# Kernel optimization log

Measured on AMD Instinct MI355X. Metric: run time of the kernel, lower is better.

Reference implementation:

```python
import jax, jax.numpy as jnp
import numpy as np

BN_EPS = 1e-5


def setup_inputs() -> dict:
    key = jax.random.key(0)
    ks = jax.random.split(key, 6)
    n, c, h, w = 16, 256, 80, 80
    mip = max(8, c // 32)  # reduction=32 -> mip=8
    x = jax.random.normal(ks[0], (n, c, h, w), dtype=jnp.float32)
    # 1x1 conv weights (bias=False), stored as [out_ch, in_ch]
    w_fc = jax.random.normal(ks[1], (mip, c), dtype=jnp.float32) * (1.0 / np.sqrt(c))
    w_h = jax.random.normal(ks[2], (c, mip), dtype=jnp.float32) * (1.0 / np.sqrt(mip))
    w_w = jax.random.normal(ks[3], (c, mip), dtype=jnp.float32) * (1.0 / np.sqrt(mip))
    # BatchNorm2d(mip) inference params
    bn_gamma = jnp.ones((mip,), dtype=jnp.float32)
    bn_beta = jnp.zeros((mip,), dtype=jnp.float32)
    bn_mean = jax.random.normal(ks[4], (mip,), dtype=jnp.float32) * 0.1
    bn_var = jax.random.uniform(ks[5], (mip,), dtype=jnp.float32, minval=0.5, maxval=1.5)
    return {"x": x, "w_fc": w_fc, "bn_gamma": bn_gamma, "bn_beta": bn_beta,
            "bn_mean": bn_mean, "bn_var": bn_var, "w_h": w_h, "w_w": w_w}


def reference(x, w_fc, bn_gamma, bn_beta, bn_mean, bn_var, w_h, w_w):
    n, c, h, w = x.shape
    # Adaptive pools: pool_h -> mean over W (n,c,h); pool_w -> mean over H (n,c,w)
    x_h = jnp.mean(x, axis=3)  # (n, c, h)
    x_w = jnp.mean(x, axis=2)  # (n, c, w)
    # concat along the length axis (equiv. to torch cat on dim=2 after permute)
    y = jnp.concatenate([x_h, x_w], axis=2)  # (n, c, h+w)
    # fc: 1x1 conv c->mip + BN (inference) + SiLU
    y = jnp.einsum('mc,ncl->nml', w_fc, y)  # (n, mip, h+w)
    inv = bn_gamma / jnp.sqrt(bn_var + BN_EPS)
    y = y * inv[None, :, None] + (bn_beta - bn_mean * inv)[None, :, None]
    y = y * jax.nn.sigmoid(y)  # SiLU
    y_h, y_w = y[:, :, :h], y[:, :, h:]  # (n, mip, h), (n, mip, w)
    a_h = jax.nn.sigmoid(jnp.einsum('cm,nml->ncl', w_h, y_h))  # (n, c, h)
    a_w = jax.nn.sigmoid(jnp.einsum('cm,nml->ncl', w_w, y_w))  # (n, c, w)
    return x * a_h[:, :, :, None] * a_w[:, :, None, :]
```

## Files before the change

kernel.cpp:

```cpp
#include <hip/hip_runtime.h>

#define N_   16
#define C_   256
#define H_   80
#define W_   80
#define MIP_ 8
#define L_   160

typedef float f32x4 __attribute__((ext_vector_type(4)));

__global__ __launch_bounds__(320) void pool_kernel(const float* __restrict__ x,
                                                   float* __restrict__ pooled) {
    __shared__ float lds_row[H_][21];
    __shared__ f32x4 lds_col[16][20];
    const int b  = blockIdx.x;
    const int t  = threadIdx.x;
    const int c4 = t % 20;
    const int rg = t / 20;

    const f32x4* xv = reinterpret_cast<const f32x4*>(x + (size_t)b * (H_ * W_));
    f32x4 colacc = {0.f, 0.f, 0.f, 0.f};
    #pragma unroll
    for (int k = 0; k < 5; ++k) {
        f32x4 q = xv[t + 320 * k];
        colacc += q;
        lds_row[rg + 16 * k][c4] = q.x + q.y + q.z + q.w;
    }
    lds_col[rg][c4] = colacc;
    __syncthreads();

    float* outp = pooled + (size_t)b * L_;
    if (t < H_) {
        float s = 0.f;
        #pragma unroll
        for (int j = 0; j < 20; ++j) s += lds_row[t][j];
        outp[t] = s * (1.0f / (float)W_);
    } else if (t >= 128 && t < 128 + 20) {
        const int j = t - 128;
        f32x4 s = lds_col[0][j];
        #pragma unroll
        for (int r = 1; r < 16; ++r) s += lds_col[r][j];
        s *= (1.0f / (float)H_);
        *reinterpret_cast<f32x4*>(outp + H_ + 4 * j) = s;
    }
}

__global__ __launch_bounds__(256) void mid_kernel(const float* __restrict__ pooled,
                                                  const float* __restrict__ w_fc,
                                                  const float* __restrict__ g,
                                                  const float* __restrict__ be,
                                                  const float* __restrict__ mu,
                                                  const float* __restrict__ va,
                                                  float* __restrict__ y_out) {
    __shared__ float red[4 * MIP_];
    const int b    = blockIdx.x;
    const int n    = b / L_;
    const int l    = b - n * L_;
    const int c    = threadIdx.x;
    const int lane = c & 63;
    const int wid  = c >> 6;

    const float p = pooled[((size_t)n * C_ + c) * L_ + l];

    #pragma unroll
    for (int m = 0; m < MIP_; ++m) {
        float v = w_fc[m * C_ + c] * p;
        #pragma unroll
        for (int off = 32; off > 0; off >>= 1) v += __shfl_down(v, off, 64);
        if (lane == 0) red[wid * MIP_ + m] = v;
    }
    __syncthreads();

    if (c < MIP_) {
        float y   = red[c] + red[MIP_ + c] + red[2 * MIP_ + c] + red[3 * MIP_ + c];
        float inv = g[c] * rsqrtf(va[c] + 1e-5f);
        y = y * inv + (be[c] - mu[c] * inv);
        y_out[(size_t)b * MIP_ + c] = y / (1.0f + expf(-y));
    }
}

__global__ __launch_bounds__(256) void apply_kernel(const float* __restrict__ x,
                                                    const float* __restrict__ y,
                                                    const float* __restrict__ w_h,
                                                    const float* __restrict__ w_w,
                                                    float* __restrict__ out) {
    __shared__ float lah[4][H_];
    __shared__ float law[4][W_];
    const int b  = blockIdx.x;
    const int n  = b >> 6;
    const int c0 = (b & 63) << 2;
    const int t  = threadIdx.x;

    #pragma unroll
    for (int pass = 0; pass < 3; ++pass) {
        int idx = t + pass * 256;
        if (idx < 4 * L_) {
            int ch = idx / L_;
            int l  = idx - ch * L_;
            int c  = c0 + ch;
            const float4* yp = reinterpret_cast<const float4*>(y + ((size_t)n * L_ + l) * MIP_);
            const float4* wp = reinterpret_cast<const float4*>(((l < H_) ? w_h : w_w) + c * MIP_);
            float4 y0 = yp[0], y1 = yp[1];
            float4 w0 = wp[0], w1 = wp[1];
            float s = y0.x * w0.x + y0.y * w0.y + y0.z * w0.z + y0.w * w0.w
                    + y1.x * w1.x + y1.y * w1.y + y1.z * w1.z + y1.w * w1.w;
            float gate = 1.0f / (1.0f + expf(-s));
            if (l < H_) lah[ch][l] = gate; else law[ch][l - H_] = gate;
        }
    }
    __syncthreads();

    const float4* xv = reinterpret_cast<const float4*>(x + ((size_t)n * C_ + c0) * (H_ * W_));
    f32x4*        ov = reinterpret_cast<f32x4*>(out + ((size_t)n * C_ + c0) * (H_ * W_));
    #pragma unroll
    for (int it = 0; it < 25; ++it) {
        int v     = t + it * 256;
        int plane = v / 1600;
        int vv    = v - plane * 1600;
        int row   = vv / 20;
        int col0  = (vv - row * 20) * 4;
        float4 q  = xv[v];
        const float ah = lah[plane][row];
        const float* lw = &law[plane][col0];
        f32x4 o;
        o.x = q.x * ah * lw[0];
        o.y = q.y * ah * lw[1];
        o.z = q.z * ah * lw[2];
        o.w = q.w * ah * lw[3];
        __builtin_nontemporal_store(o, &ov[v]);
    }
}

extern "C" void kernel_launch(void* const* d_in, const int* in_sizes, int n_in,
                              void* d_out, int out_size, void* d_ws, size_t ws_size,
                              hipStream_t stream) {
    const float* x    = (const float*)d_in[0];
    const float* w_fc = (const float*)d_in[1];
    const float* g    = (const float*)d_in[2];
    const float* be   = (const float*)d_in[3];
    const float* mu   = (const float*)d_in[4];
    const float* va   = (const float*)d_in[5];
    const float* w_h  = (const float*)d_in[6];
    const float* w_w  = (const float*)d_in[7];
    float* out = (float*)d_out;

    float* pooled = (float*)d_ws;
    float* y      = pooled + (size_t)N_ * C_ * L_;

    pool_kernel <<<N_ * C_,     320, 0, stream>>>(x, pooled);
    mid_kernel  <<<N_ * L_,     256, 0, stream>>>(pooled, w_fc, g, be, mu, va, y);
    apply_kernel<<<N_ * C_ / 4, 256, 0, stream>>>(x, y, w_h, w_w, out);
}
```

Before: 219.8 us.

## Transpose pooled buffer and compute fc per position with one thread

The pool kernel now writes pooled means transposed as [n][l][c] instead of [n][c][l]. The mid kernel changes from one block per (n,l) with shuffle reductions to one block per batch, where each thread computes all 8 fc outputs for one position by walking 256 contiguous channels with vector loads. This removes the cross-wave reductions, the shared-memory sync and the strided gather of pooled data. In exchange the pool kernel's stores become scattered, and the mid kernel launches only 16 blocks, so it may run latency-bound on very few compute units.

```diff
diff --git a/kernel.cpp b/kernel.cpp
--- a/kernel.cpp
+++ b/kernel.cpp
@@ -10,10 +10,12 @@
 typedef float f32x4 __attribute__((ext_vector_type(4)));
 
 __global__ __launch_bounds__(320) void pool_kernel(const float* __restrict__ x,
-                                                   float* __restrict__ pooled) {
+                                                   float* __restrict__ pooled_t) {
     __shared__ float lds_row[H_][21];
     __shared__ f32x4 lds_col[16][20];
     const int b  = blockIdx.x;
+    const int n  = b >> 8;
+    const int c  = b & 255;
     const int t  = threadIdx.x;
     const int c4 = t % 20;
     const int rg = t / 20;
@@ -29,54 +31,62 @@
     lds_col[rg][c4] = colacc;
     __syncthreads();
 
-    float* outp = pooled + (size_t)b * L_;
+    float* outb = pooled_t + (size_t)n * (L_ * C_) + c;
     if (t < H_) {
         float s = 0.f;
         #pragma unroll
         for (int j = 0; j < 20; ++j) s += lds_row[t][j];
-        outp[t] = s * (1.0f / (float)W_);
+        outb[t * C_] = s * (1.0f / (float)W_);
     } else if (t >= 128 && t < 128 + 20) {
         const int j = t - 128;
         f32x4 s = lds_col[0][j];
         #pragma unroll
         for (int r = 1; r < 16; ++r) s += lds_col[r][j];
         s *= (1.0f / (float)H_);
-        *reinterpret_cast<f32x4*>(outp + H_ + 4 * j) = s;
+        outb[(H_ + 4 * j    ) * C_] = s.x;
+        outb[(H_ + 4 * j + 1) * C_] = s.y;
+        outb[(H_ + 4 * j + 2) * C_] = s.z;
+        outb[(H_ + 4 * j + 3) * C_] = s.w;
     }
 }
 
-__global__ __launch_bounds__(256) void mid_kernel(const float* __restrict__ pooled,
+__global__ __launch_bounds__(192) void mid_kernel(const float* __restrict__ pooled_t,
                                                   const float* __restrict__ w_fc,
                                                   const float* __restrict__ g,
                                                   const float* __restrict__ be,
                                                   const float* __restrict__ mu,
                                                   const float* __restrict__ va,
                                                   float* __restrict__ y_out) {
-    __shared__ float red[4 * MIP_];
-    const int b    = blockIdx.x;
-    const int n    = b / L_;
-    const int l    = b - n * L_;
-    const int c    = threadIdx.x;
-    const int lane = c & 63;
-    const int wid  = c >> 6;
+    const int n = blockIdx.x;
+    const int t = threadIdx.x;
+    if (t >= L_) return;
 
-    const float p = pooled[((size_t)n * C_ + c) * L_ + l];
+    const f32x4* row = reinterpret_cast<const f32x4*>(pooled_t + ((size_t)n * L_ + t) * C_);
+    const f32x4* wv  = reinterpret_cast<const f32x4*>(w_fc);
 
+    float acc[MIP_] = {0.f, 0.f, 0.f, 0.f, 0.f, 0.f, 0.f, 0.f};
+    #pragma unroll 8
+    for (int c4 = 0; c4 < 64; ++c4) {
+        const f32x4 p = row[c4];
+        #pragma unroll
+        for (int m = 0; m < MIP_; ++m) {
+            const f32x4 w4 = wv[m * 64 + c4];
+            acc[m] += p.x * w4.x + p.y * w4.y + p.z * w4.z + p.w * w4.w;
+        }
+    }
+
+    f32x4 o0, o1;
     #pragma unroll
     for (int m = 0; m < MIP_; ++m) {
-        float v = w_fc[m * C_ + c] * p;
-        #pragma unroll
-        for (int off = 32; off > 0; off >>= 1) v += __shfl_down(v, off, 64);
-        if (lane == 0) red[wid * MIP_ + m] = v;
+        const float inv = g[m] * rsqrtf(va[m] + 1e-5f);
+        float s = acc[m] * inv + (be[m] - mu[m] * inv);
+        s = s / (1.0f + expf(-s));
+        if (m < 4) { (m == 0) ? (o0.x = s) : (m == 1) ? (o0.y = s) : (m == 2) ? (o0.z = s) : (o0.w = s); }
+        else       { (m == 4) ? (o1.x = s) : (m == 5) ? (o1.y = s) : (m == 6) ? (o1.z = s) : (o1.w = s); }
     }
-    __syncthreads();
-
-    if (c < MIP_) {
-        float y   = red[c] + red[MIP_ + c] + red[2 * MIP_ + c] + red[3 * MIP_ + c];
-        float inv = g[c] * rsqrtf(va[c] + 1e-5f);
-        y = y * inv + (be[c] - mu[c] * inv);
-        y_out[(size_t)b * MIP_ + c] = y / (1.0f + expf(-y));
-    }
+    f32x4* yp = reinterpret_cast<f32x4*>(y_out + ((size_t)n * L_ + t) * MIP_);
+    yp[0] = o0;
+    yp[1] = o1;
 }
 
 __global__ __launch_bounds__(256) void apply_kernel(const float* __restrict__ x,
@@ -144,10 +154,10 @@
     const float* w_w  = (const float*)d_in[7];
     float* out = (float*)d_out;
 
-    float* pooled = (float*)d_ws;
-    float* y      = pooled + (size_t)N_ * C_ * L_;
+    float* pooled_t = (float*)d_ws;
+    float* y        = pooled_t + (size_t)N_ * L_ * C_;
 
-    pool_kernel <<<N_ * C_,     320, 0, stream>>>(x, pooled);
-    mid_kernel  <<<N_ * L_,     256, 0, stream>>>(pooled, w_fc, g, be, mu, va, y);
+    pool_kernel <<<N_ * C_,     320, 0, stream>>>(x, pooled_t);
+    mid_kernel  <<<N_,          192, 0, stream>>>(pooled_t, w_fc, g, be, mu, va, y);
     apply_kernel<<<N_ * C_ / 4, 256, 0, stream>>>(x, y, w_h, w_w, out);
 }
```

After: 245.9 us. +11.9%, slower.
